# Kernel optimization log

Hardware: AMD Instinct MI355X
Metric: run time of the kernel (lower is better)

The kernel has to match this reference:

```python
import jax, jax.numpy as jnp
import numpy as np

B, NV, JN = 1024, 8, 21
V = NV * JN            # 168 tokens = num_view * joint_num
F_DIM, NH, DQ, DV = 512, 4, 128, 128
HID = 512
EPS = 1e-6
NEG = float(-2**32 + 1)


def _layer_norm(x, g, b):
    mu = jnp.mean(x, axis=-1, keepdims=True)
    var = jnp.mean(jnp.square(x - mu), axis=-1, keepdims=True)
    return (x - mu) * jax.lax.rsqrt(var + EPS) * g + b


def setup_inputs() -> dict:
    key = jax.random.key(0)
    ks = jax.random.split(key, 12)
    s = 0.02
    return {
        "x": jax.random.normal(ks[0], (B, V, F_DIM), dtype=jnp.float32),
        "valid": jax.random.randint(ks[1], (B, NV), 0, 2),
        "wq": jax.random.normal(ks[2], (NH * DQ, F_DIM), dtype=jnp.float32) * s,
        "bq": jnp.zeros((NH * DQ,), dtype=jnp.float32),
        "wk": jax.random.normal(ks[3], (NH * DQ, F_DIM), dtype=jnp.float32) * s,
        "bk": jnp.zeros((NH * DQ,), dtype=jnp.float32),
        "wv": jax.random.normal(ks[4], (NH * DV, F_DIM), dtype=jnp.float32) * s,
        "bv": jnp.zeros((NH * DV,), dtype=jnp.float32),
        "fc_w": jax.random.normal(ks[5], (F_DIM, NH * DV), dtype=jnp.float32) * s,
        "fc_b": jnp.zeros((F_DIM,), dtype=jnp.float32),
        "ln1_g": jnp.ones((F_DIM,), dtype=jnp.float32),
        "ln1_b": jnp.zeros((F_DIM,), dtype=jnp.float32),
        "ln2_g": jnp.ones((F_DIM,), dtype=jnp.float32),
        "ln2_b": jnp.zeros((F_DIM,), dtype=jnp.float32),
        "fc1_w": jax.random.normal(ks[6], (HID, F_DIM), dtype=jnp.float32) * s,
        "fc1_b": jnp.zeros((HID,), dtype=jnp.float32),
        "fc2_w": jax.random.normal(ks[7], (F_DIM, HID), dtype=jnp.float32) * s,
        "fc2_b": jnp.zeros((F_DIM,), dtype=jnp.float32),
    }


def reference(x, valid, wq, bq, wk, bk, wv, bv, fc_w, fc_b,
              ln1_g, ln1_b, ln2_g, ln2_b, fc1_w, fc1_b, fc2_w, fc2_b):
    bs = x.shape[0]
    h = _layer_norm(x, ln1_g, ln1_b)                          # [B,V,f]
    q = (h @ wq.T + bq).reshape(bs, V, NH, DQ)                # [B,V,H,dq]
    k = (h @ wk.T + bk).reshape(bs, V, NH, DQ)
    v = (h @ wv.T + bv).reshape(bs, V, NH, DV)
    attn = jnp.einsum('bqhd,bkhd->bhqk', q, k) / jnp.sqrt(jnp.float32(DQ))
    # valid mask: per-view validity expanded to per-token, pairwise additive
    w = jnp.where(valid == 0, NEG, 0.0).astype(x.dtype)       # [B,NV]
    w = jnp.repeat(w, JN, axis=1)                             # [B,V], view-major
    m = w[:, :, None] + w[:, None, :]                         # [B,V,V]
    attn = attn + m[:, None, :, :]
    attn = jax.nn.softmax(attn, axis=-1)
    out = jnp.einsum('bhqk,bkhd->bqhd', attn, v).reshape(bs, V, NH * DV)
    out = out @ fc_w.T + fc_b
    x = x + out
    # MLP residual block
    h2 = _layer_norm(x, ln2_g, ln2_b)
    h2 = jax.nn.relu(h2 @ fc1_w.T + fc1_b) @ fc2_w.T + fc2_b
    return x + h2
```

## Files before the change

kernel.cpp:

```cpp
#include <hip/hip_runtime.h>
#include <stdint.h>

#define BATCH 1024
#define NVIEW 8
#define JN_   21
#define VTOK  168
#define FDIM  512
#define NHEAD 4
#define DHEAD 128
#define MROWS (BATCH*VTOK)
#define SCALE2 0.127517434f

typedef __attribute__((ext_vector_type(8))) short s8v;
typedef __attribute__((ext_vector_type(4))) short s4v;
typedef __attribute__((ext_vector_type(4))) float f4v;

static __device__ __forceinline__ short f2bf(float f){
  unsigned u = __builtin_bit_cast(unsigned, f);
  unsigned r = (u + 0x7FFFu + ((u >> 16) & 1u)) >> 16;
  return (short)(unsigned short)r;
}
static __device__ __forceinline__ float bf2f(short s){
  unsigned u = ((unsigned)(unsigned short)s) << 16;
  return __builtin_bit_cast(float, u);
}

#define GL16(gp, lp) __builtin_amdgcn_global_load_lds( \
    (__attribute__((address_space(1))) void*)(gp), \
    (__attribute__((address_space(3))) void*)(lp), 16, 0, 0)

__global__ __launch_bounds__(256) void convert_w(
    const float* __restrict__ wq, const float* __restrict__ wk,
    const float* __restrict__ wv, const float* __restrict__ fcw,
    const float* __restrict__ fc1, const float* __restrict__ fc2,
    short* __restrict__ dst){
  int id = blockIdx.x * 256 + threadIdx.x;
  int e = id * 4;
  int seg = e >> 18;
  int off = e & 262143;
  const float* s = seg==0?wq: seg==1?wk: seg==2?wv: seg==3?fcw: seg==4?fc1: fc2;
  float4 u = *(const float4*)(s + off);
  s4v o; o[0]=f2bf(u.x); o[1]=f2bf(u.y); o[2]=f2bf(u.z); o[3]=f2bf(u.w);
  *(s4v*)(dst + e) = o;
}

__global__ __launch_bounds__(256) void ln1_kernel(
    const float* __restrict__ x, const float* __restrict__ g,
    const float* __restrict__ bb, short* __restrict__ h){
  int row  = blockIdx.x * 4 + (threadIdx.x >> 6);
  int lane = threadIdx.x & 63;
  size_t base = (size_t)row * 512 + lane * 8;
  float4 u0 = *(const float4*)(x + base);
  float4 u1 = *(const float4*)(x + base + 4);
  float s = u0.x+u0.y+u0.z+u0.w + u1.x+u1.y+u1.z+u1.w;
  float q = u0.x*u0.x+u0.y*u0.y+u0.z*u0.z+u0.w*u0.w
          + u1.x*u1.x+u1.y*u1.y+u1.z*u1.z+u1.w*u1.w;
  #pragma unroll
  for (int o = 1; o < 64; o <<= 1){ s += __shfl_xor(s,o); q += __shfl_xor(q,o); }
  float mu = s * (1.f/512.f);
  float rstd = rsqrtf(q*(1.f/512.f) - mu*mu + 1e-6f);
  float4 g0 = *(const float4*)(g + lane*8),  g1 = *(const float4*)(g + lane*8 + 4);
  float4 b0 = *(const float4*)(bb + lane*8), b1 = *(const float4*)(bb + lane*8 + 4);
  s8v o_;
  o_[0]=f2bf((u0.x-mu)*rstd*g0.x+b0.x); o_[1]=f2bf((u0.y-mu)*rstd*g0.y+b0.y);
  o_[2]=f2bf((u0.z-mu)*rstd*g0.z+b0.z); o_[3]=f2bf((u0.w-mu)*rstd*g0.w+b0.w);
  o_[4]=f2bf((u1.x-mu)*rstd*g1.x+b1.x); o_[5]=f2bf((u1.y-mu)*rstd*g1.y+b1.y);
  o_[6]=f2bf((u1.z-mu)*rstd*g1.z+b1.z); o_[7]=f2bf((u1.w-mu)*rstd*g1.w+b1.w);
  *(s8v*)(h + base) = o_;
}

__global__ __launch_bounds__(256) void resid_ln(
    const float* __restrict__ x, const short* __restrict__ y,
    const float* __restrict__ g, const float* __restrict__ bb,
    short* __restrict__ x2b, short* __restrict__ g2){
  int row  = blockIdx.x * 4 + (threadIdx.x >> 6);
  int lane = threadIdx.x & 63;
  size_t base = (size_t)row * 512 + lane * 8;
  float4 u0 = *(const float4*)(x + base);
  float4 u1 = *(const float4*)(x + base + 4);
  s8v yv = *(const s8v*)(y + base);
  float v[8];
  v[0]=u0.x+bf2f(yv[0]); v[1]=u0.y+bf2f(yv[1]); v[2]=u0.z+bf2f(yv[2]); v[3]=u0.w+bf2f(yv[3]);
  v[4]=u1.x+bf2f(yv[4]); v[5]=u1.y+bf2f(yv[5]); v[6]=u1.z+bf2f(yv[6]); v[7]=u1.w+bf2f(yv[7]);
  s8v xv;
  #pragma unroll
  for (int i = 0; i < 8; i++) xv[i] = f2bf(v[i]);
  *(s8v*)(x2b + base) = xv;
  float s = 0.f, q = 0.f;
  #pragma unroll
  for (int i = 0; i < 8; i++){ s += v[i]; q += v[i]*v[i]; }
  #pragma unroll
  for (int o = 1; o < 64; o <<= 1){ s += __shfl_xor(s,o); q += __shfl_xor(q,o); }
  float mu = s * (1.f/512.f);
  float rstd = rsqrtf(q*(1.f/512.f) - mu*mu + 1e-6f);
  float4 g0 = *(const float4*)(g + lane*8),  g1 = *(const float4*)(g + lane*8 + 4);
  float4 b0 = *(const float4*)(bb + lane*8), b1 = *(const float4*)(bb + lane*8 + 4);
  s8v o_;
  o_[0]=f2bf((v[0]-mu)*rstd*g0.x+b0.x); o_[1]=f2bf((v[1]-mu)*rstd*g0.y+b0.y);
  o_[2]=f2bf((v[2]-mu)*rstd*g0.z+b0.z); o_[3]=f2bf((v[3]-mu)*rstd*g0.w+b0.w);
  o_[4]=f2bf((v[4]-mu)*rstd*g1.x+b1.x); o_[5]=f2bf((v[5]-mu)*rstd*g1.y+b1.y);
  o_[6]=f2bf((v[6]-mu)*rstd*g1.z+b1.z); o_[7]=f2bf((v[7]-mu)*rstd*g1.w+b1.w);
  *(s8v*)(g2 + base) = o_;
}

template<int MODE>
__global__ __launch_bounds__(512, 1) void gemm_bt(
    const short* __restrict__ A, const short* __restrict__ Bm,
    const float* __restrict__ bias0, const float* __restrict__ bias1,
    const short* __restrict__ aux, short* __restrict__ out0,
    short* __restrict__ out1, float* __restrict__ outf){
  __shared__ short lds[81920];
  short* const AL = lds;
  short* const BL = lds + 49152;
  const int tid = threadIdx.x, lane = tid & 63;
  const int wid = tid >> 6, wr = wid >> 2, wc = wid & 3;
  const int lg = lane >> 4, l15 = lane & 15, l7 = lane & 7;
  const int nwg  = gridDim.x * gridDim.y;
  const int flat = blockIdx.y * gridDim.x + blockIdx.x;
  const int swz  = (flat & 7) * (nwg >> 3) + (flat >> 3);
  size_t mt, nt;
  if (MODE == 1){ mt = swz & 1; nt = (size_t)(swz >> 1); }
  else {
    constexpr int GX = (MODE == 0) ? 4 : 2;
    nt = swz % GX; mt = swz / GX;
  }
  const size_t m0 = mt * 256, n0 = nt * 256;
  const short* Ab = A + m0 * 512;
  const short* Bb = Bm + n0 * 512;

#define STAGEA(slot, tile, half) do {                                   \
    const short* s_ = Ab + (size_t)(half)*65536 + (tile)*64;            \
    short* d_ = AL + (slot)*8192;                                       \
    _Pragma("unroll")                                                   \
    for (int r_ = 0; r_ < 2; r_++){                                     \
      int c_ = r_*512 + tid;                                            \
      int row_ = c_ >> 3, chk_ = (c_ & 7) ^ (row_ & 7);                 \
      GL16(s_ + (size_t)row_*512 + chk_*8, d_ + c_*8);                  \
    } } while(0)
#define STAGEB(slot, tile, half) do {                                   \
    const short* s_ = Bb + (size_t)(half)*65536 + (tile)*64;            \
    short* d_ = BL + (slot)*8192;                                       \
    _Pragma("unroll")                                                   \
    for (int r_ = 0; r_ < 2; r_++){                                     \
      int c_ = r_*512 + tid;                                            \
      int row_ = c_ >> 3, chk_ = (c_ & 7) ^ (row_ & 7);                 \
      GL16(s_ + (size_t)row_*512 + chk_*8, d_ + c_*8);                  \
    } } while(0)

  STAGEA(0, 0, 0); STAGEA(1, 0, 1);
  STAGEB(0, 0, 0); STAGEB(1, 0, 1);
  STAGEA(2, 1, 0); STAGEA(3, 1, 1);
  asm volatile("s_waitcnt vmcnt(4)" ::: "memory");
  __builtin_amdgcn_s_barrier();

  f4v acc[8][4];
  #pragma unroll
  for (int m=0;m<8;m++)
    #pragma unroll
    for (int n=0;n<4;n++) acc[m][n] = f4v{0.f,0.f,0.f,0.f};

  s8v a0[8], b0[4];
  #pragma unroll
  for (int t = 0; t < 8; ++t){
    const short* Awp = AL + ((2*t)%6 + wr)*8192 + l15*64;
    const short* Bwp = BL + ((2*t)%4 + (wc>>1))*8192 + ((wc&1)*64 + l15)*64;
    const int c0 = (lg ^ l7) * 8;
    const int c1 = ((4 + lg) ^ l7) * 8;
    #pragma unroll
    for (int n=0;n<4;n++) b0[n] = *(const s8v*)(Bwp + n*1024 + c0);
    #pragma unroll
    for (int m=0;m<8;m++) a0[m] = *(const s8v*)(Awp + m*1024 + c0);
    if (t < 7){ STAGEB((2*t+2)%4, t+1, 0); STAGEB((2*t+2)%4 + 1, t+1, 1); }
    __builtin_amdgcn_s_setprio(1);
    #pragma unroll
    for (int m=0;m<8;m++)
      #pragma unroll
      for (int n=0;n<4;n++)
        acc[m][n] = __builtin_amdgcn_mfma_f32_16x16x32_bf16(a0[m], b0[n], acc[m][n], 0,0,0);
    __builtin_amdgcn_s_setprio(0);
    #pragma unroll
    for (int n=0;n<4;n++) b0[n] = *(const s8v*)(Bwp + n*1024 + c1);
    #pragma unroll
    for (int m=0;m<8;m++) a0[m] = *(const s8v*)(Awp + m*1024 + c1);
    if (t < 6){ STAGEA((2*t+4)%6, t+2, 0); STAGEA((2*t+4)%6 + 1, t+2, 1); }
    __builtin_amdgcn_s_setprio(1);
    #pragma unroll
    for (int m=0;m<8;m++)
      #pragma unroll
      for (int n=0;n<4;n++)
        acc[m][n] = __builtin_amdgcn_mfma_f32_16x16x32_bf16(a0[m], b0[n], acc[m][n], 0,0,0);
    __builtin_amdgcn_s_setprio(0);
    if (t < 6)       asm volatile("s_waitcnt vmcnt(4)" ::: "memory");
    else if (t == 6) asm volatile("s_waitcnt vmcnt(0)" ::: "memory");
    __builtin_amdgcn_s_barrier();
  }
#undef STAGEA
#undef STAGEB

  #pragma unroll
  for (int m=0;m<8;m++)
  #pragma unroll
  for (int n=0;n<4;n++)
  #pragma unroll
  for (int r=0;r<4;r++){
    int rowL = wr*128 + m*16 + lg*4 + r;
    int colL = wc*64 + n*16 + l15;
    size_t gm = m0 + rowL, gn = n0 + colL;
    float val = acc[m][n][r];
    if (MODE == 0){
      int nn = (int)gn;
      val += (nn < 512) ? bias0[nn] : bias1[nn - 512];
      int head = (nn >> 7) & 3, d = nn & 127;
      size_t b = gm / 168, tok = gm - b * 168;
      size_t idx = ((b*4 + head)*168 + tok)*128 + d;
      ((nn < 512) ? out0 : out1)[idx] = f2bf(val);
    } else if (MODE == 1){
      val += bias0[gm];
      int hh = ((int)gm >> 7) & 3, d = (int)gm & 127;
      size_t b = gn / 168, tok = gn - b * 168;
      out0[((b*4 + hh)*128 + d)*168 + tok] = f2bf(val);
    } else if (MODE == 2 || MODE == 3){
      val += bias0[gn];
      if (MODE == 3) val = fmaxf(val, 0.f);
      out0[gm*512 + gn] = f2bf(val);
    } else {
      val += bias0[gn] + bf2f(aux[gm*512 + gn]);
      outf[gm*512 + gn] = val;
    }
  }
}

__global__ __launch_bounds__(256, 2) void attn_kernel(
    const short* __restrict__ qg_, const short* __restrict__ kg_,
    const short* __restrict__ vtg_, const int* __restrict__ valid,
    short* __restrict__ outp){
  __shared__ short ldsb[38400];
  short* const Kl = ldsb;
  short* const Ps = ldsb;

  int tid = threadIdx.x, lane = tid & 63, wid = tid >> 6;
  int lg = lane >> 4, l15 = lane & 15;
  int bh = blockIdx.x, b = bh >> 2, hh = bh & 3;
  const short* qg  = qg_  + (size_t)bh * (168*128);
  const short* kg  = kg_  + (size_t)bh * (168*128);
  const short* vtg = vtg_ + (size_t)bh * (128*168);

  #pragma unroll
  for (int r = 0; r < 11; r++){
    int c = r*256 + tid;
    int row = c >> 4;
    int g = (c & 15) ^ ((row & 1) << 2);
    GL16(kg + (size_t)row*128 + g*8, Kl + c*8);
  }

  int bits = 0;
  #pragma unroll
  for (int v = 0; v < 8; v++) bits |= (valid[b*8 + v] != 0) << v;
  if (bits == 0) bits = 255;
  float wk2[11];
  #pragma unroll
  for (int n = 0; n < 11; n++){
    int kt = n*16 + l15;
    int view = (kt * 781) >> 14;
    wk2[n] = ((bits >> view) & 1) ? 0.0f : -1.0e9f;
  }

  int row0 = wid * 48;
  f4v zf = {0.f,0.f,0.f,0.f};

  s8v qf[3][4];
  #pragma unroll
  for (int m=0;m<3;m++)
    #pragma unroll
    for (int kf=0;kf<4;kf++)
      qf[m][kf] = *(const s8v*)(qg + (size_t)(row0 + m*16 + l15)*128 + kf*32 + lg*8);

  asm volatile("s_waitcnt vmcnt(0)" ::: "memory");
  __builtin_amdgcn_s_barrier();

  f4v accS[3][11];
  #pragma unroll
  for (int m=0;m<3;m++)
    #pragma unroll
    for (int n=0;n<11;n++) accS[m][n] = zf;
  #pragma unroll
  for (int n=0;n<11;n++){
    s8v kb[4];
    #pragma unroll
    for (int kf=0;kf<4;kf++)
      kb[kf] = *(const s8v*)&Kl[(size_t)(n*16 + l15)*128 + (((kf*4 + lg) ^ ((l15 & 1) << 2)) << 3)];
    __builtin_amdgcn_s_setprio(1);
    #pragma unroll
    for (int kf=0;kf<4;kf++)
      #pragma unroll
      for (int m=0;m<3;m++)
        accS[m][n] = __builtin_amdgcn_mfma_f32_16x16x32_bf16(qf[m][kf], kb[kf], accS[m][n], 0,0,0);
    __builtin_amdgcn_s_setprio(0);
  }
  __builtin_amdgcn_s_barrier();

  float inv_[3][4];
  #pragma unroll
  for (int m=0;m<3;m++){
    #pragma unroll
    for (int r=0;r<4;r++){
      int qtok = row0 + m*16 + lg*4 + r;
      float sum = 0.f;
      #pragma unroll
      for (int n=0;n<11;n++){
        float p = exp2f(fmaf(accS[m][n][r], SCALE2, wk2[n]));
        sum += p;
        Ps[qtok*200 + n*16 + l15] = f2bf(p);
      }
      sum += __shfl_xor(sum,1); sum += __shfl_xor(sum,2);
      sum += __shfl_xor(sum,4); sum += __shfl_xor(sum,8);
      inv_[m][r] = 1.0f / sum;
    }
  }
  {
    s8v z8 = {0,0,0,0,0,0,0,0};
    for (int i = lane; i < 96; i += 64){
      int rr = row0 + (i >> 1);
      *(s8v*)&Ps[rr*200 + 176 + (i&1)*8] = z8;
    }
  }

  s8v ap[3][6];
  #pragma unroll
  for (int m=0;m<3;m++)
    #pragma unroll
    for (int kf=0;kf<6;kf++)
      ap[m][kf] = *(const s8v*)&Ps[(row0 + m*16 + l15)*200 + kf*32 + lg*8];

  f4v accO[3][8];
  #pragma unroll
  for (int m=0;m<3;m++)
    #pragma unroll
    for (int n=0;n<8;n++) accO[m][n] = zf;
  s8v vb[3][6];
  #pragma unroll
  for (int p=0;p<2;p++)
    #pragma unroll
    for (int kf=0;kf<6;kf++)
      vb[p][kf] = *(const s8v*)(vtg + (size_t)(p*16 + l15)*168 + kf*32 + lg*8);
  #pragma unroll
  for (int n=0;n<8;n++){
    if (n < 6){
      #pragma unroll
      for (int kf=0;kf<6;kf++)
        vb[(n+2)%3][kf] = *(const s8v*)(vtg + (size_t)((n+2)*16 + l15)*168 + kf*32 + lg*8);
    }
    __builtin_amdgcn_s_setprio(1);
    #pragma unroll
    for (int kf=0;kf<6;kf++)
      #pragma unroll
      for (int m=0;m<3;m++)
        accO[m][n] = __builtin_amdgcn_mfma_f32_16x16x32_bf16(ap[m][kf], vb[n%3][kf], accO[m][n], 0,0,0);
    __builtin_amdgcn_s_setprio(0);
  }

  #pragma unroll
  for (int m=0;m<3;m++){
    #pragma unroll
    for (int r=0;r<4;r++){
      int qtok = row0 + m*16 + lg*4 + r;
      if (qtok < 168){
        float iv = inv_[m][r];
        size_t base = ((size_t)b*168 + qtok)*512 + hh*128;
        #pragma unroll
        for (int n=0;n<8;n++)
          outp[base + n*16 + l15] = f2bf(accO[m][n][r] * iv);
      }
    }
  }
}

extern "C" void kernel_launch(void* const* d_in, const int* in_sizes, int n_in,
                              void* d_out, int out_size, void* d_ws, size_t ws_size,
                              hipStream_t stream) {
  const float* x     = (const float*)d_in[0];
  const int*   valid = (const int*)  d_in[1];
  const float* wq    = (const float*)d_in[2];
  const float* bq    = (const float*)d_in[3];
  const float* wk    = (const float*)d_in[4];
  const float* bk    = (const float*)d_in[5];
  const float* wv    = (const float*)d_in[6];
  const float* bv    = (const float*)d_in[7];
  const float* fcw   = (const float*)d_in[8];
  const float* fcb   = (const float*)d_in[9];
  const float* ln1g  = (const float*)d_in[10];
  const float* ln1b  = (const float*)d_in[11];
  const float* ln2g  = (const float*)d_in[12];
  const float* ln2b  = (const float*)d_in[13];
  const float* fc1w  = (const float*)d_in[14];
  const float* fc1b  = (const float*)d_in[15];
  const float* fc2w  = (const float*)d_in[16];
  const float* fc2b  = (const float*)d_in[17];

  char* ws = (char*)d_ws;
  short* h       = (short*)(ws + 0LL);
  short* q_ws    = (short*)(ws + 176160768LL);
  short* k_ws    = (short*)(ws + 352321536LL);
  short* vt_ws   = (short*)(ws + 528482304LL);
  short* wb      = (short*)(ws + 704643072LL);
  short* attn_o  = h;
  short* y       = q_ws;
  short* g2      = h;
  short* a1      = k_ws;
  short* x2b     = vt_ws;
  float* outp    = (float*)d_out;

  convert_w<<<1536, 256, 0, stream>>>(wq, wk, wv, fcw, fc1w, fc2w, wb);
  ln1_kernel<<<MROWS/4, 256, 0, stream>>>(x, ln1g, ln1b, h);
  gemm_bt<0><<<dim3(4, MROWS/256), 512, 0, stream>>>(h, wb, bq, bk, nullptr, q_ws, k_ws, nullptr);
  gemm_bt<1><<<dim3(2, MROWS/256), 512, 0, stream>>>(wb + 524288, h, bv, nullptr, nullptr, vt_ws, nullptr, nullptr);
  attn_kernel<<<BATCH*NHEAD, 256, 0, stream>>>(q_ws, k_ws, vt_ws, valid, attn_o);
  gemm_bt<2><<<dim3(2, MROWS/256), 512, 0, stream>>>(attn_o, wb + 786432, fcb, nullptr, nullptr, y, nullptr, nullptr);
  resid_ln<<<MROWS/4, 256, 0, stream>>>(x, y, ln2g, ln2b, x2b, g2);
  gemm_bt<3><<<dim3(2, MROWS/256), 512, 0, stream>>>(g2, wb + 1048576, fc1b, nullptr, nullptr, a1, nullptr, nullptr);
  gemm_bt<4><<<dim3(2, MROWS/256), 512, 0, stream>>>(a1, wb + 1310720, fc2b, nullptr, x2b, nullptr, nullptr, outp);
}
```

Measured before the change: 1.242 ms.

## Load weight operand directly to registers instead of staging through LDS in GEMM

The GEMM kernel no longer stages the weight (B) tile through shared memory. Each wave now loads its B fragments straight from global memory into a triple-buffered register ring, and only the activation tile is staged in LDS, with a full 256-row tile per slot. The V projection is changed to use the same orientation as the other GEMMs, with activations as A and weights as B, and the epilogue writes the transposed V layout from that. This reduces LDS footprint and traffic, but adds per-wave global loads of weights, more register pressure, and the vmcnt wait counts now have to match the new load counts.

```diff
diff --git a/kernel.cpp b/kernel.cpp
--- a/kernel.cpp
+++ b/kernel.cpp
@@ -105,52 +105,46 @@
 
 template<int MODE>
 __global__ __launch_bounds__(512, 1) void gemm_bt(
-    const short* __restrict__ A, const short* __restrict__ Bm,
+    const short* __restrict__ A, const short* __restrict__ Wm,
     const float* __restrict__ bias0, const float* __restrict__ bias1,
     const short* __restrict__ aux, short* __restrict__ out0,
     short* __restrict__ out1, float* __restrict__ outf){
-  __shared__ short lds[81920];
-  short* const AL = lds;
-  short* const BL = lds + 49152;
+  __shared__ short AL[49152];
   const int tid = threadIdx.x, lane = tid & 63;
   const int wid = tid >> 6, wr = wid >> 2, wc = wid & 3;
   const int lg = lane >> 4, l15 = lane & 15, l7 = lane & 7;
   const int nwg  = gridDim.x * gridDim.y;
   const int flat = blockIdx.y * gridDim.x + blockIdx.x;
   const int swz  = (flat & 7) * (nwg >> 3) + (flat >> 3);
-  size_t mt, nt;
-  if (MODE == 1){ mt = swz & 1; nt = (size_t)(swz >> 1); }
-  else {
-    constexpr int GX = (MODE == 0) ? 4 : 2;
-    nt = swz % GX; mt = swz / GX;
-  }
+  constexpr int GX = (MODE == 0) ? 4 : 2;
+  const size_t nt = swz % GX, mt = swz / GX;
   const size_t m0 = mt * 256, n0 = nt * 256;
   const short* Ab = A + m0 * 512;
-  const short* Bb = Bm + n0 * 512;
-
-#define STAGEA(slot, tile, half) do {                                   \
-    const short* s_ = Ab + (size_t)(half)*65536 + (tile)*64;            \
-    short* d_ = AL + (slot)*8192;                                       \
+
+  const short* wp0 = Wm + (n0 + (size_t)wc*64 +  0 + l15)*512 + lg*8;
+  const short* wp1 = Wm + (n0 + (size_t)wc*64 + 16 + l15)*512 + lg*8;
+  const short* wp2 = Wm + (n0 + (size_t)wc*64 + 32 + l15)*512 + lg*8;
+  const short* wp3 = Wm + (n0 + (size_t)wc*64 + 48 + l15)*512 + lg*8;
+
+#define STAGEA(tt) do {                                                 \
+    short* d_ = AL + ((tt)%3)*16384;                                    \
     _Pragma("unroll")                                                   \
-    for (int r_ = 0; r_ < 2; r_++){                                     \
+    for (int r_ = 0; r_ < 4; r_++){                                     \
       int c_ = r_*512 + tid;                                            \
       int row_ = c_ >> 3, chk_ = (c_ & 7) ^ (row_ & 7);                 \
-      GL16(s_ + (size_t)row_*512 + chk_*8, d_ + c_*8);                  \
+      GL16(Ab + (size_t)row_*512 + (tt)*64 + chk_*8, d_ + c_*8);        \
     } } while(0)
-#define STAGEB(slot, tile, half) do {                                   \
-    const short* s_ = Bb + (size_t)(half)*65536 + (tile)*64;            \
-    short* d_ = BL + (slot)*8192;                                       \
-    _Pragma("unroll")                                                   \
-    for (int r_ = 0; r_ < 2; r_++){                                     \
-      int c_ = r_*512 + tid;                                            \
-      int row_ = c_ >> 3, chk_ = (c_ & 7) ^ (row_ & 7);                 \
-      GL16(s_ + (size_t)row_*512 + chk_*8, d_ + c_*8);                  \
-    } } while(0)
-
-  STAGEA(0, 0, 0); STAGEA(1, 0, 1);
-  STAGEB(0, 0, 0); STAGEB(1, 0, 1);
-  STAGEA(2, 1, 0); STAGEA(3, 1, 1);
-  asm volatile("s_waitcnt vmcnt(4)" ::: "memory");
+#define LOADB(dst, s) do {                                              \
+    (dst)[0] = *(const s8v*)(wp0 + (s)*32);                             \
+    (dst)[1] = *(const s8v*)(wp1 + (s)*32);                             \
+    (dst)[2] = *(const s8v*)(wp2 + (s)*32);                             \
+    (dst)[3] = *(const s8v*)(wp3 + (s)*32); } while(0)
+
+  s8v breg[3][4];
+  STAGEA(0); STAGEA(1);
+  LOADB(breg[0], 0);
+  LOADB(breg[1], 1);
+  asm volatile("s_waitcnt vmcnt(12)" ::: "memory");
   __builtin_amdgcn_s_barrier();
 
   f4v acc[8][4];
@@ -159,43 +153,39 @@
     #pragma unroll
     for (int n=0;n<4;n++) acc[m][n] = f4v{0.f,0.f,0.f,0.f};
 
-  s8v a0[8], b0[4];
+  s8v a0[8];
   #pragma unroll
   for (int t = 0; t < 8; ++t){
-    const short* Awp = AL + ((2*t)%6 + wr)*8192 + l15*64;
-    const short* Bwp = BL + ((2*t)%4 + (wc>>1))*8192 + ((wc&1)*64 + l15)*64;
+    const short* Awp = AL + (t%3)*16384 + (wr*128 + l15)*64;
     const int c0 = (lg ^ l7) * 8;
     const int c1 = ((4 + lg) ^ l7) * 8;
-    #pragma unroll
-    for (int n=0;n<4;n++) b0[n] = *(const s8v*)(Bwp + n*1024 + c0);
+    if (2*t+2 < 16) LOADB(breg[(2*t+2)%3], 2*t+2);
     #pragma unroll
     for (int m=0;m<8;m++) a0[m] = *(const s8v*)(Awp + m*1024 + c0);
-    if (t < 7){ STAGEB((2*t+2)%4, t+1, 0); STAGEB((2*t+2)%4 + 1, t+1, 1); }
     __builtin_amdgcn_s_setprio(1);
     #pragma unroll
     for (int m=0;m<8;m++)
       #pragma unroll
       for (int n=0;n<4;n++)
-        acc[m][n] = __builtin_amdgcn_mfma_f32_16x16x32_bf16(a0[m], b0[n], acc[m][n], 0,0,0);
+        acc[m][n] = __builtin_amdgcn_mfma_f32_16x16x32_bf16(a0[m], breg[(2*t)%3][n], acc[m][n], 0,0,0);
     __builtin_amdgcn_s_setprio(0);
-    #pragma unroll
-    for (int n=0;n<4;n++) b0[n] = *(const s8v*)(Bwp + n*1024 + c1);
+    if (2*t+3 < 16) LOADB(breg[(2*t+3)%3], 2*t+3);
+    if (t < 6) STAGEA(t+2);
     #pragma unroll
     for (int m=0;m<8;m++) a0[m] = *(const s8v*)(Awp + m*1024 + c1);
-    if (t < 6){ STAGEA((2*t+4)%6, t+2, 0); STAGEA((2*t+4)%6 + 1, t+2, 1); }
     __builtin_amdgcn_s_setprio(1);
     #pragma unroll
     for (int m=0;m<8;m++)
       #pragma unroll
       for (int n=0;n<4;n++)
-        acc[m][n] = __builtin_amdgcn_mfma_f32_16x16x32_bf16(a0[m], b0[n], acc[m][n], 0,0,0);
+        acc[m][n] = __builtin_amdgcn_mfma_f32_16x16x32_bf16(a0[m], breg[(2*t+1)%3][n], acc[m][n], 0,0,0);
     __builtin_amdgcn_s_setprio(0);
     if (t < 6)       asm volatile("s_waitcnt vmcnt(4)" ::: "memory");
     else if (t == 6) asm volatile("s_waitcnt vmcnt(0)" ::: "memory");
     __builtin_amdgcn_s_barrier();
   }
 #undef STAGEA
-#undef STAGEB
+#undef LOADB
 
   #pragma unroll
   for (int m=0;m<8;m++)
@@ -215,10 +205,10 @@
       size_t idx = ((b*4 + head)*168 + tok)*128 + d;
       ((nn < 512) ? out0 : out1)[idx] = f2bf(val);
     } else if (MODE == 1){
-      val += bias0[gm];
-      int hh = ((int)gm >> 7) & 3, d = (int)gm & 127;
-      size_t b = gn / 168, tok = gn - b * 168;
-      out0[((b*4 + hh)*128 + d)*168 + tok] = f2bf(val);
+      val += bias0[gn];
+      int hh = ((int)gn >> 7) & 3, d = (int)gn & 127;
+      size_t b = gm / 168, tok = gm - b * 168;
+      out0[(((size_t)b*4 + hh)*128 + d)*168 + tok] = f2bf(val);
     } else if (MODE == 2 || MODE == 3){
       val += bias0[gn];
       if (MODE == 3) val = fmaxf(val, 0.f);
@@ -413,7 +403,7 @@
   convert_w<<<1536, 256, 0, stream>>>(wq, wk, wv, fcw, fc1w, fc2w, wb);
   ln1_kernel<<<MROWS/4, 256, 0, stream>>>(x, ln1g, ln1b, h);
   gemm_bt<0><<<dim3(4, MROWS/256), 512, 0, stream>>>(h, wb, bq, bk, nullptr, q_ws, k_ws, nullptr);
-  gemm_bt<1><<<dim3(2, MROWS/256), 512, 0, stream>>>(wb + 524288, h, bv, nullptr, nullptr, vt_ws, nullptr, nullptr);
+  gemm_bt<1><<<dim3(2, MROWS/256), 512, 0, stream>>>(h, wb + 524288, bv, nullptr, nullptr, vt_ws, nullptr, nullptr);
   attn_kernel<<<BATCH*NHEAD, 256, 0, stream>>>(q_ws, k_ws, vt_ws, valid, attn_o);
   gemm_bt<2><<<dim3(2, MROWS/256), 512, 0, stream>>>(attn_o, wb + 786432, fcb, nullptr, nullptr, y, nullptr, nullptr);
   resid_ln<<<MROWS/4, 256, 0, stream>>>(x, y, ln2g, ln2b, x2b, g2);
```

After: 1.632 ms. 1.31x slower.
